# Performance work log

Measured on AMD Instinct MI355X. Metric: run time of the kernel, lower is better.

Reference implementation:

```python
import jax, jax.numpy as jnp
import numpy as np

NQ = 10
EDGES = [[0, 1], [1, 2], [2, 3], [3, 4], [4, 5], [5, 6], [6, 7], [7, 8], [8, 9], [9, 0]]
RANGE = 2  # StronglyEntanglingLayers ranges=[2]
CRX_ANGLE = np.pi / 3.0  # trainBool=False -> constant angle

_c, _s = np.cos(CRX_ANGLE / 2), np.sin(CRX_ANGLE / 2)
CRX = np.array([[1, 0, 0, 0], [0, 1, 0, 0], [0, 0, _c, -1j * _s], [0, 0, -1j * _s, _c]], dtype=np.complex64)
CNOT = np.array([[1, 0, 0, 0], [0, 1, 0, 0], [0, 0, 0, 1], [0, 0, 1, 0]], dtype=np.complex64)


def _apply_1q(state, U, w):
    # state: (B, 2, ..., 2); U: (2,2) or batched (B,2,2)
    st = jnp.moveaxis(state, 1 + w, -1)
    if U.ndim == 3:
        st = jnp.einsum('b...i,bji->b...j', st, U)
    else:
        st = jnp.einsum('...i,ji->...j', st, U)
    return jnp.moveaxis(st, -1, 1 + w)


def _apply_2q(state, U, w1, w2):
    st = jnp.moveaxis(state, (1 + w1, 1 + w2), (-2, -1))
    shp = st.shape
    st = st.reshape(shp[:-2] + (4,))
    st = jnp.einsum('...i,ji->...j', st, U)
    return jnp.moveaxis(st.reshape(shp), (-2, -1), (1 + w1, 1 + w2))


def _ry_batch(theta):
    # per-sample RY gates, theta: (B,) -> (B,2,2)
    c, s = jnp.cos(theta / 2), jnp.sin(theta / 2)
    U = jnp.stack([jnp.stack([c, -s], -1), jnp.stack([s, c], -1)], -2)
    return U.astype(jnp.complex64)


def _rot(phi, theta, omega):
    # qml.Rot = RZ(omega) RY(theta) RZ(phi)
    c, s = jnp.cos(theta / 2), jnp.sin(theta / 2)
    u00 = jnp.exp(-0.5j * (phi + omega)) * c
    u01 = -jnp.exp(0.5j * (phi - omega)) * s
    u10 = jnp.exp(-0.5j * (phi - omega)) * s
    u11 = jnp.exp(0.5j * (phi + omega)) * c
    return jnp.stack([jnp.stack([u00, u01]), jnp.stack([u10, u11])]).astype(jnp.complex64)


def _circuit(inputs, weights):
    B = inputs.shape[0]
    state = jnp.zeros((B,) + (2,) * NQ, jnp.complex64)
    state = state.at[(slice(None),) + (0,) * NQ].set(1.0)
    # AngleEmbedding(rotation='Y')
    for w in range(NQ):
        state = _apply_1q(state, _ry_batch(inputs[:, w]), w)
    # CRX entanglers over the chain graph, angle pi/3
    for a, b in EDGES:
        state = _apply_2q(state, CRX, a, b)
    # StronglyEntanglingLayers, n_layers = weights.shape[0] = 1, range 2
    for l in range(weights.shape[0]):
        for i in range(NQ):
            state = _apply_1q(state, _rot(weights[l, i, 0], weights[l, i, 1], weights[l, i, 2]), i)
        for i in range(NQ):
            state = _apply_2q(state, CNOT, i, (i + RANGE) % NQ)
    # expval(PauliZ(i)) for each wire
    probs = state.real ** 2 + state.imag ** 2
    exps = []
    for i in range(NQ):
        axes = tuple(a for a in range(1, NQ + 1) if a != 1 + i)
        marg = probs.sum(axis=axes)  # (B, 2)
        exps.append(marg[:, 0] - marg[:, 1])
    return jnp.stack(exps, -1)  # (B, NQ)


def setup_inputs() -> dict:
    key = jax.random.key(0)
    k1, k2 = jax.random.split(key)
    inputs = jax.random.normal(k1, (8192, NQ), dtype=jnp.float32)
    weights = jax.random.uniform(k2, (1, NQ, 3), dtype=jnp.float32, minval=0.0, maxval=2 * np.pi)
    return {"inputs": inputs, "weights": weights}


def reference(inputs, weights):
    return _circuit(inputs, weights)
```

## Files before the change

### kernel.cpp

```cpp
#include <hip/hip_runtime.h>

#define NQ 10

typedef float f32x2 __attribute__((ext_vector_type(2)));
struct cplx2 { f32x2 x, y; };

template<int M>
__device__ __forceinline__ void plswap1(float v, float &A, float &B){
    if constexpr (M == 16) {
        auto r = __builtin_amdgcn_permlane16_swap(__float_as_uint(v), __float_as_uint(v), false, false);
        A = __uint_as_float(r[0]); B = __uint_as_float(r[1]);
    } else {
        auto r = __builtin_amdgcn_permlane32_swap(__float_as_uint(v), __float_as_uint(v), false, false);
        A = __uint_as_float(r[0]); B = __uint_as_float(r[1]);
    }
}
template<int M>
__device__ __forceinline__ void plswap2(f32x2 v, f32x2 &A, f32x2 &B){
    float ax, bx, ay, by;
    plswap1<M>(v.x, ax, bx);
    plswap1<M>(v.y, ay, by);
    A.x = ax; A.y = ay;
    B.x = bx; B.y = by;
}

template<int M>
__device__ __forceinline__ float lxf(float v){
    if constexpr (M == 1 || M == 2 || M == 8) {
        constexpr int ctrl = (M == 1) ? 0xB1 : (M == 2) ? 0x4E : 0x128;
        return __int_as_float(__builtin_amdgcn_update_dpp(
            0, __float_as_int(v), ctrl, 0xF, 0xF, true));
    } else if constexpr (M == 4) {
        float up = __int_as_float(__builtin_amdgcn_update_dpp(
            0, __float_as_int(v), 0x104, 0xF, 0xF, true));
        float dn = __int_as_float(__builtin_amdgcn_update_dpp(
            0, __float_as_int(v), 0x114, 0xF, 0xF, true));
        return (threadIdx.x & 4) ? dn : up;
    } else {
        float A, Bv; plswap1<M>(v, A, Bv);
        return (threadIdx.x & M) ? A : Bv;
    }
}
template<int M>
__device__ __forceinline__ f32x2 lx2(f32x2 v){
    f32x2 r; r.x = lxf<M>(v.x); r.y = lxf<M>(v.y); return r;
}
template<int M>
__device__ __forceinline__ cplx2 lxc(cplx2 a){
    cplx2 r; r.x = lx2<M>(a.x); r.y = lx2<M>(a.y); return r;
}

template<int M, int R>
__device__ __forceinline__ void rot_reg(cplx2 (&a)[16],
        float u00x,float u00y,float u01x,float u01y,
        float u10x,float u10y,float u11x,float u11y){
    if constexpr (R < 16) {
        if constexpr ((R & M) == 0) {
            cplx2 a0 = a[R], a1 = a[R|M];
            a[R].x   = u00x*a0.x - u00y*a0.y + u01x*a1.x - u01y*a1.y;
            a[R].y   = u00x*a0.y + u00y*a0.x + u01x*a1.y + u01y*a1.x;
            a[R|M].x = u10x*a0.x - u10y*a0.y + u11x*a1.x - u11y*a1.y;
            a[R|M].y = u10x*a0.y + u10y*a0.x + u11x*a1.y + u11y*a1.x;
        }
        rot_reg<M,R+1>(a, u00x,u00y,u01x,u01y,u10x,u10y,u11x,u11y);
    }
}

template<int LM, int R>
__device__ __forceinline__ void rot_lane(cplx2 (&a)[16],
        float uax,float uay,float ubx,float uby){
    if constexpr (R < 16) {
        cplx2 p = lxc<LM>(a[R]);
        cplx2 m = a[R];
        a[R].x = uax*m.x - uay*m.y + ubx*p.x - uby*p.y;
        a[R].y = uax*m.y + uay*m.x + ubx*p.y + uby*p.x;
        rot_lane<LM,R+1>(a, uax,uay,ubx,uby);
    }
}

template<int M, int R>
__device__ __forceinline__ void rot_lane_pl(cplx2 (&a)[16],
        float vax,float vay,float vbx,float vby){
    if constexpr (R < 16) {
        f32x2 Ax,Bx,Ay,By;
        plswap2<M>(a[R].x, Ax, Bx);
        plswap2<M>(a[R].y, Ay, By);
        a[R].x = vax*Ax - vay*Ay + vbx*Bx - vby*By;
        a[R].y = vax*Ay + vay*Ax + vbx*By + vby*Bx;
        rot_lane_pl<M,R+1>(a, vax,vay,vbx,vby);
    }
}


template<int MC, int MT, int R>
__device__ __forceinline__ void crx_rr(cplx2 (&a)[16], float cc, float ss){
    if constexpr (R < 16) {
        if constexpr ((R & MC) != 0 && (R & MT) == 0) {
            cplx2 a0 = a[R], a1 = a[R|MT];
            a[R].x    = cc*a0.x + ss*a1.y;  a[R].y    = cc*a0.y - ss*a1.x;
            a[R|MT].x = cc*a1.x + ss*a0.y;  a[R|MT].y = cc*a1.y - ss*a0.x;
        }
        crx_rr<MC,MT,R+1>(a, cc, ss);
    }
}

template<int MC, int LM, int R>
__device__ __forceinline__ void crx_rl(cplx2 (&a)[16], float cc, float ss){
    if constexpr (R < 16) {
        if constexpr ((R & MC) != 0) {
            cplx2 p = lxc<LM>(a[R]);
            cplx2 m = a[R];
            a[R].x = cc*m.x + ss*p.y;
            a[R].y = cc*m.y - ss*p.x;
        }
        crx_rl<MC,LM,R+1>(a, cc, ss);
    }
}

template<int MT, int R>
__device__ __forceinline__ void crx_lr(cplx2 (&a)[16], float al, float be){
    if constexpr (R < 16) {
        if constexpr ((R & MT) == 0) {
            cplx2 a0 = a[R], a1 = a[R|MT];
            a[R].x    = al*a0.x + be*a1.y;  a[R].y    = al*a0.y - be*a1.x;
            a[R|MT].x = al*a1.x + be*a0.y;  a[R|MT].y = al*a1.y - be*a0.x;
        }
        crx_lr<MT,R+1>(a, al, be);
    }
}

template<int TLM, int R>
__device__ __forceinline__ void crx_ll(cplx2 (&a)[16], float al, float be){
    if constexpr (R < 16) {
        cplx2 p = lxc<TLM>(a[R]);
        cplx2 m = a[R];
        a[R].x = al*m.x + be*p.y;
        a[R].y = al*m.y - be*p.x;
        crx_ll<TLM,R+1>(a, al, be);
    }
}

template<int M, int R>
__device__ __forceinline__ void crx_ll_pl(cplx2 (&a)[16],
        float kmA,float kmB,float kpA,float kpB){
    if constexpr (R < 16) {
        f32x2 Ax,Bx,Ay,By;
        plswap2<M>(a[R].x, Ax, Bx);
        plswap2<M>(a[R].y, Ay, By);
        a[R].x = kmA*Ax + kmB*Bx + kpA*Ay + kpB*By;
        a[R].y = kmA*Ay + kmB*By - kpA*Ax - kpB*Bx;
        crx_ll_pl<M,R+1>(a, kmA,kmB,kpA,kpB);
    }
}

template<int I>
__device__ __forceinline__ void do_rot(cplx2 (&amp)[16], int lane, const float* __restrict__ w){
    float phi = w[I*3 + 0], th = w[I*3 + 1];
    float ct, st, cp, sp;
    __sincosf(0.5f * th,  &st, &ct);
    __sincosf(0.5f * phi, &sp, &cp);
    float A = ct*cp, Bv = ct*sp, C = st*cp, D = st*sp;
    if constexpr (I < 4) {
        rot_reg<(1<<I),0>(amp, A,-Bv, -C,-D, C,-D, A,Bv);
    } else if constexpr (I < 8) {
        constexpr int LM = 1 << (I - 4);
        const bool hi = (lane & LM) != 0;
        float uax = A,            uay = hi ? Bv : -Bv;
        float ubx = hi ? C : -C,  uby = -D;
        rot_lane<LM,0>(amp, uax,uay,ubx,uby);
    } else {
        constexpr int LM = 1 << (I - 4);
        const bool hi = (lane & LM) != 0;
        float vax = hi ? C  : A;
        float vay = hi ? -D : -Bv;
        float vbx = hi ? A  : -C;
        float vby = hi ? Bv : -D;
        rot_lane_pl<LM,0>(amp, vax,vay,vbx,vby);
    }
}

template<int R>
__device__ __forceinline__ void accum4(const cplx2 (&a)[16], f32x2 &SA, f32x2 &SB, f32x2 &SC, f32x2 &SD){
    if constexpr (R < 16) {
        f32x2 p = a[R].x*a[R].x + a[R].y*a[R].y;
        SA += ((R>>2) & 1)            ? -p : p;
        SB += ((R>>3) & 1)            ? -p : p;
        SC += ((R ^ (R>>2)) & 1)      ? -p : p;
        SD += (((R>>1) ^ (R>>3)) & 1) ? -p : p;
        accum4<R+1>(a, SA, SB, SC, SD);
    }
}

__device__ __forceinline__ f32x2 wave_sum2(f32x2 v){
    v += lx2< 1>(v);
    v += lx2< 2>(v);
    v += lx2< 4>(v);
    v += lx2< 8>(v);
    f32x2 A, B;
    plswap2<16>(v, A, B); v = A + B;
    plswap2<32>(v, A, B); v = A + B;
    return v;
}

__device__ __forceinline__ f32x2 wht2(f32x2 v, int lane){
    f32x2 p;
    p = lx2< 1>(v); v = (lane &  1) ? p - v : v + p;
    p = lx2< 2>(v); v = (lane &  2) ? p - v : v + p;
    p = lx2< 4>(v); v = (lane &  4) ? p - v : v + p;
    p = lx2< 8>(v); v = (lane &  8) ? p - v : v + p;
    f32x2 A, B;
    plswap2<16>(v, A, B); v = (lane & 16) ? A - B : A + B;
    plswap2<32>(v, A, B); v = (lane & 32) ? A - B : A + B;
    return v;
}

__device__ __forceinline__ f32x2 fsgn2(f32x2 v, unsigned s){
    f32x2 r;
    r.x = __uint_as_float(__float_as_uint(v.x) ^ s);
    r.y = __uint_as_float(__float_as_uint(v.y) ^ s);
    return r;
}
__device__ __forceinline__ unsigned parsgn(int lane, int m){
    return (unsigned)((__builtin_popcount(lane & m) & 1)) << 31;
}

__global__ __launch_bounds__(256, 4) void qsim_kernel(const float* __restrict__ inputs,
                                                      const float* __restrict__ weights,
                                                      float* __restrict__ out, int B, int nPairs){
    const int lane = threadIdx.x & 63;
    const int pair = __builtin_amdgcn_readfirstlane((int)((blockIdx.x * blockDim.x + threadIdx.x) >> 6));
    if (pair >= nPairs) return;

    const int s0 = 2 * pair;
    const int s1 = (s0 + 1 < B) ? s0 + 1 : s0;
    const float* ang0 = inputs + (size_t)s0 * NQ;
    const float* ang1 = inputs + (size_t)s1 * NQ;

    f32x2 F = 1.f;
    #pragma unroll
    for (int w = 4; w < NQ; ++w) {
        float sA, cA, sB, cB;
        __sincosf(0.5f * ang0[w], &sA, &cA);
        __sincosf(0.5f * ang1[w], &sB, &cB);
        bool hi = (lane & (1 << (w - 4))) != 0;
        f32x2 f; f.x = hi ? sA : cA; f.y = hi ? sB : cB;
        F *= f;
    }

    f32x2 c[4], s[4];
    #pragma unroll
    for (int w = 0; w < 4; ++w) {
        float sA, cA, sB, cB;
        __sincosf(0.5f * ang0[w], &sA, &cA);
        __sincosf(0.5f * ang1[w], &sB, &cB);
        c[w].x = cA; c[w].y = cB; s[w].x = sA; s[w].y = sB;
    }

    f32x2 v2a = F * c[0], v2b = F * s[0];
    f32x2 v4[4] = { v2a*c[1], v2b*c[1], v2a*s[1], v2b*s[1] };
    f32x2 v8[8] = { v4[0]*c[2], v4[1]*c[2], v4[2]*c[2], v4[3]*c[2],
                    v4[0]*s[2], v4[1]*s[2], v4[2]*s[2], v4[3]*s[2] };

    cplx2 amp[16];
    #pragma unroll
    for (int r = 0; r < 8; ++r) {
        amp[r].x   = v8[r] * c[3]; amp[r].y   = 0.f;
        amp[r+8].x = v8[r] * s[3]; amp[r+8].y = 0.f;
    }

    const float cc = 0.86602540378443864676f;
    const float ss = 0.5f;
    crx_rr<1, 2, 0>(amp, cc, ss);
    crx_rr<2, 4, 0>(amp, cc, ss);
    crx_rr<4, 8, 0>(amp, cc, ss);
    crx_rl<8, 1, 0>(amp, cc, ss);
    { bool t = (lane &  1); crx_ll< 2,0>(amp, t?cc:1.f, t?ss:0.f); }
    { bool t = (lane &  2); crx_ll< 4,0>(amp, t?cc:1.f, t?ss:0.f); }
    { bool t = (lane &  4); crx_ll< 8,0>(amp, t?cc:1.f, t?ss:0.f); }
    { bool t = (lane &  8); bool bt = (lane & 16);
      float al = t?cc:1.f, be = t?ss:0.f;
      crx_ll_pl<16,0>(amp, bt?0.f:al, bt?al:0.f, bt?be:0.f, bt?0.f:be); }
    { bool t = (lane & 16); bool bt = (lane & 32);
      float al = t?cc:1.f, be = t?ss:0.f;
      crx_ll_pl<32,0>(amp, bt?0.f:al, bt?al:0.f, bt?be:0.f, bt?0.f:be); }
    { bool t = (lane & 32); crx_lr< 1,0>(amp, t?cc:1.f, t?ss:0.f); }

    do_rot<0>(amp, lane, weights);
    do_rot<1>(amp, lane, weights);
    do_rot<2>(amp, lane, weights);
    do_rot<3>(amp, lane, weights);
    do_rot<4>(amp, lane, weights);
    do_rot<5>(amp, lane, weights);
    do_rot<6>(amp, lane, weights);
    do_rot<7>(amp, lane, weights);
    do_rot<8>(amp, lane, weights);
    do_rot<9>(amp, lane, weights);

    f32x2 SA = 0.f, SB = 0.f, SC = 0.f, SD = 0.f;
    accum4<0>(amp, SA, SB, SC, SD);

    f32x2 r0  = wave_sum2(fsgn2(SA, parsgn(lane, 21)));
    f32x2 r1  = wave_sum2(fsgn2(SB, parsgn(lane, 42)));
    f32x2 wsc = wht2(SC, lane);
    f32x2 wsd = wht2(SD, lane);

    float* o0 = out + (size_t)s0 * NQ;
    const bool has1 = (s0 + 1 < B);
    float* o1 = out + (size_t)(s0 + 1) * NQ;

    if (lane == 0) {
        o0[0] = r0.x; o0[1] = r1.x; o0[2] = wsc.x; o0[3] = wsd.x;
        if (has1) { o1[0] = r0.y; o1[1] = r1.y; o1[2] = wsc.y; o1[3] = wsd.y; }
    } else if (lane == 1) {
        o0[4] = wsc.x; if (has1) o1[4] = wsc.y;
    } else if (lane == 5) {
        o0[6] = wsc.x; if (has1) o1[6] = wsc.y;
    } else if (lane == 21) {
        o0[8] = wsc.x; if (has1) o1[8] = wsc.y;
    } else if (lane == 2) {
        o0[5] = wsd.x; if (has1) o1[5] = wsd.y;
    } else if (lane == 10) {
        o0[7] = wsd.x; if (has1) o1[7] = wsd.y;
    } else if (lane == 42) {
        o0[9] = wsd.x; if (has1) o1[9] = wsd.y;
    }
}

extern "C" void kernel_launch(void* const* d_in, const int* in_sizes, int n_in,
                              void* d_out, int out_size, void* d_ws, size_t ws_size,
                              hipStream_t stream) {
    const float* inputs  = (const float*)d_in[0];
    const float* weights = (const float*)d_in[1];
    float* out = (float*)d_out;
    const int B = in_sizes[0] / NQ;
    const int nPairs = (B + 1) / 2;
    const int wavesPerBlock = 256 / 64;
    const int blocks = (nPairs + wavesPerBlock - 1) / wavesPerBlock;
    qsim_kernel<<<blocks, 256, 0, stream>>>(inputs, weights, out, B, nPairs);
}
```

Before: 84.15 us.

## Factor Rot gates into one diagonal phase pass plus real RY rotations

Rewrites the final layer of Rot gates by pulling the RZ(phi) factors out as a single diagonal phase applied to every amplitude, and drops RZ(omega) since it does not change measured probabilities. The remaining per-qubit rotations become real RY mixes with half the multiplies of the complex 2x2 updates. This adds a precomputed phase table and one complex multiply per amplitude, and relies on the diagonal phases commuting before the RY gates.

```diff
diff --git a/kernel.cpp b/kernel.cpp
--- a/kernel.cpp
+++ b/kernel.cpp
@@ -51,43 +51,37 @@
 }
 
 template<int M, int R>
-__device__ __forceinline__ void rot_reg(cplx2 (&a)[16],
-        float u00x,float u00y,float u01x,float u01y,
-        float u10x,float u10y,float u11x,float u11y){
+__device__ __forceinline__ void ry_reg(cplx2 (&a)[16], float c, float s){
     if constexpr (R < 16) {
         if constexpr ((R & M) == 0) {
             cplx2 a0 = a[R], a1 = a[R|M];
-            a[R].x   = u00x*a0.x - u00y*a0.y + u01x*a1.x - u01y*a1.y;
-            a[R].y   = u00x*a0.y + u00y*a0.x + u01x*a1.y + u01y*a1.x;
-            a[R|M].x = u10x*a0.x - u10y*a0.y + u11x*a1.x - u11y*a1.y;
-            a[R|M].y = u10x*a0.y + u10y*a0.x + u11x*a1.y + u11y*a1.x;
-        }
-        rot_reg<M,R+1>(a, u00x,u00y,u01x,u01y,u10x,u10y,u11x,u11y);
+            a[R].x   = c*a0.x - s*a1.x;  a[R].y   = c*a0.y - s*a1.y;
+            a[R|M].x = s*a0.x + c*a1.x;  a[R|M].y = s*a0.y + c*a1.y;
+        }
+        ry_reg<M,R+1>(a, c, s);
     }
 }
 
 template<int LM, int R>
-__device__ __forceinline__ void rot_lane(cplx2 (&a)[16],
-        float uax,float uay,float ubx,float uby){
+__device__ __forceinline__ void ry_lane(cplx2 (&a)[16], float c, float se){
     if constexpr (R < 16) {
         cplx2 p = lxc<LM>(a[R]);
         cplx2 m = a[R];
-        a[R].x = uax*m.x - uay*m.y + ubx*p.x - uby*p.y;
-        a[R].y = uax*m.y + uay*m.x + ubx*p.y + uby*p.x;
-        rot_lane<LM,R+1>(a, uax,uay,ubx,uby);
+        a[R].x = c*m.x + se*p.x;
+        a[R].y = c*m.y + se*p.y;
+        ry_lane<LM,R+1>(a, c, se);
     }
 }
 
 template<int M, int R>
-__device__ __forceinline__ void rot_lane_pl(cplx2 (&a)[16],
-        float vax,float vay,float vbx,float vby){
+__device__ __forceinline__ void ry_lane_pl(cplx2 (&a)[16], float kA, float kB){
     if constexpr (R < 16) {
         f32x2 Ax,Bx,Ay,By;
         plswap2<M>(a[R].x, Ax, Bx);
         plswap2<M>(a[R].y, Ay, By);
-        a[R].x = vax*Ax - vay*Ay + vbx*Bx - vby*By;
-        a[R].y = vax*Ay + vay*Ax + vbx*By + vby*Bx;
-        rot_lane_pl<M,R+1>(a, vax,vay,vbx,vby);
+        a[R].x = kA*Ax + kB*Bx;
+        a[R].y = kA*Ay + kB*By;
+        ry_lane_pl<M,R+1>(a, kA, kB);
     }
 }
 
@@ -154,28 +148,19 @@
 }
 
 template<int I>
-__device__ __forceinline__ void do_rot(cplx2 (&amp)[16], int lane, const float* __restrict__ w){
-    float phi = w[I*3 + 0], th = w[I*3 + 1];
-    float ct, st, cp, sp;
-    __sincosf(0.5f * th,  &st, &ct);
-    __sincosf(0.5f * phi, &sp, &cp);
-    float A = ct*cp, Bv = ct*sp, C = st*cp, D = st*sp;
+__device__ __forceinline__ void do_ry(cplx2 (&amp)[16], int lane, const float* __restrict__ w){
+    float c, s;
+    __sincosf(0.5f * w[I*3 + 1], &s, &c);
     if constexpr (I < 4) {
-        rot_reg<(1<<I),0>(amp, A,-Bv, -C,-D, C,-D, A,Bv);
+        ry_reg<(1<<I),0>(amp, c, s);
     } else if constexpr (I < 8) {
         constexpr int LM = 1 << (I - 4);
         const bool hi = (lane & LM) != 0;
-        float uax = A,            uay = hi ? Bv : -Bv;
-        float ubx = hi ? C : -C,  uby = -D;
-        rot_lane<LM,0>(amp, uax,uay,ubx,uby);
+        ry_lane<LM,0>(amp, c, hi ? s : -s);
     } else {
         constexpr int LM = 1 << (I - 4);
         const bool hi = (lane & LM) != 0;
-        float vax = hi ? C  : A;
-        float vay = hi ? -D : -Bv;
-        float vbx = hi ? A  : -C;
-        float vby = hi ? Bv : -D;
-        rot_lane_pl<LM,0>(amp, vax,vay,vbx,vby);
+        ry_lane_pl<LM,0>(amp, hi ? s : c, hi ? c : -s);
     }
 }
 
@@ -285,16 +270,57 @@
       crx_ll_pl<32,0>(amp, bt?0.f:al, bt?al:0.f, bt?be:0.f, bt?0.f:be); }
     { bool t = (lane & 32); crx_lr< 1,0>(amp, t?cc:1.f, t?ss:0.f); }
 
-    do_rot<0>(amp, lane, weights);
-    do_rot<1>(amp, lane, weights);
-    do_rot<2>(amp, lane, weights);
-    do_rot<3>(amp, lane, weights);
-    do_rot<4>(amp, lane, weights);
-    do_rot<5>(amp, lane, weights);
-    do_rot<6>(amp, lane, weights);
-    do_rot<7>(amp, lane, weights);
-    do_rot<8>(amp, lane, weights);
-    do_rot<9>(amp, lane, weights);
+    {
+        float cp[NQ], sp[NQ];
+        #pragma unroll
+        for (int i = 0; i < NQ; ++i)
+            __sincosf(0.5f * weights[i*3 + 0], &sp[i], &cp[i]);
+
+        float Lr = 1.f, Li = 0.f;
+        #pragma unroll
+        for (int wq = 4; wq < NQ; ++wq) {
+            float sg = (lane & (1 << (wq - 4))) ? sp[wq] : -sp[wq];
+            float nr = Lr*cp[wq] - Li*sg;
+            float ni = Li*cp[wq] + Lr*sg;
+            Lr = nr; Li = ni;
+        }
+
+        float er[8], ei[8];
+        er[0] = Lr; ei[0] = Li;
+        #pragma unroll
+        for (int q = 0; q < 3; ++q) {
+            const int n = 1 << q;
+            #pragma unroll
+            for (int r = n - 1; r >= 0; --r) {
+                float ar = er[r], ai = ei[r];
+                er[r+n] = ar*cp[q] - ai*sp[q];
+                ei[r+n] = ai*cp[q] + ar*sp[q];
+                er[r]   = ar*cp[q] + ai*sp[q];
+                ei[r]   = ai*cp[q] - ar*sp[q];
+            }
+        }
+        #pragma unroll
+        for (int r = 0; r < 8; ++r) {
+            float g0r = er[r]*cp[3] + ei[r]*sp[3], g0i = ei[r]*cp[3] - er[r]*sp[3];
+            float g1r = er[r]*cp[3] - ei[r]*sp[3], g1i = ei[r]*cp[3] + er[r]*sp[3];
+            f32x2 x, y;
+            x = amp[r].x;   y = amp[r].y;
+            amp[r].x   = x*g0r - y*g0i;  amp[r].y   = y*g0r + x*g0i;
+            x = amp[r+8].x; y = amp[r+8].y;
+            amp[r+8].x = x*g1r - y*g1i;  amp[r+8].y = y*g1r + x*g1i;
+        }
+    }
+
+    do_ry<0>(amp, lane, weights);
+    do_ry<1>(amp, lane, weights);
+    do_ry<2>(amp, lane, weights);
+    do_ry<3>(amp, lane, weights);
+    do_ry<4>(amp, lane, weights);
+    do_ry<5>(amp, lane, weights);
+    do_ry<6>(amp, lane, weights);
+    do_ry<7>(amp, lane, weights);
+    do_ry<8>(amp, lane, weights);
+    do_ry<9>(amp, lane, weights);
 
     f32x2 SA = 0.f, SB = 0.f, SC = 0.f, SD = 0.f;
     accum4<0>(amp, SA, SB, SC, SD);
```

Measured after the change: 80.22 us (median of 2 runs). 4.7% less time.
